# Optimization experiments

Hardware: AMD Instinct MI355X
Metric: run time of the kernel (lower is better)

## Reference

```python
import jax, jax.numpy as jnp
import numpy as np

BINS = 256


def _equalize_uint8(flat):
    """Torchvision-style histogram equalization.
    flat: int32 [BC, HW] with values in [0, 255]. Returns int32 [BC, HW]."""
    BC, HW = flat.shape
    # per-(image,channel) 256-bin histogram via one fused scatter-add
    ids = (flat + BINS * jnp.arange(BC, dtype=jnp.int32)[:, None]).reshape(-1)
    hist = jax.ops.segment_sum(
        jnp.ones((BC * HW,), dtype=jnp.int32), ids, num_segments=BC * BINS
    ).reshape(BC, BINS)
    # count in the last nonzero bin (torchvision: nonzero_hist[:-1].sum() = total - last)
    nz = hist > 0
    last_idx = (BINS - 1) - jnp.argmax(nz[:, ::-1], axis=1)
    last = jnp.take_along_axis(hist, last_idx[:, None], axis=1)[:, 0]
    step = (HW - last) // (BINS - 1)  # floor div by 255
    # lut = floor((cumsum(hist) + step//2) / step), shifted right by one, clamped
    cum = jnp.cumsum(hist, axis=1)
    safe_step = jnp.maximum(step, 1)[:, None]
    lut = (cum + (step // 2)[:, None]) // safe_step
    lut = jnp.clip(
        jnp.concatenate([jnp.zeros((BC, 1), jnp.int32), lut[:, :-1]], axis=1), 0, BINS - 1
    )
    eq = jnp.take_along_axis(lut, flat, axis=1)
    # step == 0 -> identity channel
    return jnp.where((step == 0)[:, None], flat, eq)


def setup_inputs() -> dict:
    key = jax.random.key(0)
    x = jax.random.uniform(key, (64, 3, 512, 512), dtype=jnp.float32)
    return {"x": x}


def reference(x) -> jnp.ndarray:
    B, C, H, W = x.shape
    # (x * 255).byte(): truncation toward zero == floor for non-negative inputs
    img = jnp.clip(jnp.floor(x * 255.0), 0.0, 255.0).astype(jnp.int32)
    flat = img.reshape(B * C, H * W)
    eq = _equalize_uint8(flat)
    return (eq.reshape(B, C, H, W).astype(x.dtype)) / 255.0
```

## Files before the change

kernel.cpp:

```cpp
#include <hip/hip_runtime.h>

#define BINS 256
#define HWPIX (512 * 512)
#define NCH 192
#define BPC 32
#define NBLK (NCH * BPC)

#define PWS_BYTES    ((size_t)NBLK * BINS * sizeof(int))
#define STAGED_BYTES ((size_t)NCH * HWPIX)

typedef float f4v __attribute__((ext_vector_type(4)));


__global__ __launch_bounds__(256) void hist_stage(const float* __restrict__ x,
                                                  int* __restrict__ pws,
                                                  uint4* __restrict__ staged4) {
    __shared__ int h[BINS];
    const int t = threadIdx.x;
    h[t] = 0;
    __syncthreads();

    const int ch  = blockIdx.x >> 5;
    const int blk = blockIdx.x & 31;
    const f4v* in4 = (const f4v*)(x + (size_t)ch * HWPIX);
    uint4* st4 = staged4 + (size_t)ch * (BPC * 512) + (size_t)blk * 512;
    const int idx0 = blk * 2048 + t;

#pragma unroll
    for (int j = 0; j < 2; ++j) {
        unsigned int p[4];
#pragma unroll
        for (int m = 0; m < 4; ++m) {
            const int k = idx0 + (4 * j + m) * 256;
            f4v v = in4[k];
            int b0 = (int)fminf(fmaxf(floorf(v.x * 255.0f), 0.0f), 255.0f);
            int b1 = (int)fminf(fmaxf(floorf(v.y * 255.0f), 0.0f), 255.0f);
            int b2 = (int)fminf(fmaxf(floorf(v.z * 255.0f), 0.0f), 255.0f);
            int b3 = (int)fminf(fmaxf(floorf(v.w * 255.0f), 0.0f), 255.0f);
            p[m] = (unsigned int)b0 | ((unsigned int)b1 << 8) |
                   ((unsigned int)b2 << 16) | ((unsigned int)b3 << 24);
            atomicAdd(&h[b0], 1);
            atomicAdd(&h[b1], 1);
            atomicAdd(&h[b2], 1);
            atomicAdd(&h[b3], 1);
        }
        uint4 w;
        w.x = p[0]; w.y = p[1]; w.z = p[2]; w.w = p[3];
        st4[j * 256 + t] = w;
    }
    __syncthreads();
    pws[(size_t)blockIdx.x * BINS + t] = h[t];
}

__global__ __launch_bounds__(256) void lut_kernel(const int* __restrict__ pws,
                                                  float* __restrict__ glut) {
    __shared__ int h[BINS];
    __shared__ int cum[BINS];
    __shared__ int red[BINS];
    const int t = threadIdx.x;
    const int ch = blockIdx.x;

    const int* base = pws + (size_t)ch * BPC * BINS;
    int s = 0;
#pragma unroll
    for (int b = 0; b < BPC; ++b) s += base[b * BINS + t];
    h[t]   = s;
    cum[t] = s;
    red[t] = (s > 0) ? t : -1;
    __syncthreads();

    for (int off = 128; off > 0; off >>= 1) {
        if (t < off) red[t] = max(red[t], red[t + off]);
        __syncthreads();
    }
    for (int off = 1; off < BINS; off <<= 1) {
        int v = cum[t];
        int a = (t >= off) ? cum[t - off] : 0;
        __syncthreads();
        cum[t] = v + a;
        __syncthreads();
    }

    const int last = h[red[0]];
    const int step = (HWPIX - last) / 255;
    int lutv;
    if (step == 0) {
        lutv = t;
    } else if (t == 0) {
        lutv = 0;
    } else {
        int val = (cum[t - 1] + (step >> 1)) / step;
        lutv = min(max(val, 0), 255);
    }
    glut[ch * BINS + t] = (float)lutv / 255.0f;
}

__global__ __launch_bounds__(256) void apply_staged(const uint4* __restrict__ staged4,
                                                    const float* __restrict__ glut,
                                                    float* __restrict__ out) {
    __shared__ float lutf[BINS];
    const int t = threadIdx.x;
    const int ch  = blockIdx.x >> 5;
    const int blk = blockIdx.x & 31;

    lutf[t] = glut[ch * BINS + t];
    __syncthreads();

    const uint4* st4 = staged4 + (size_t)ch * (BPC * 512) + (size_t)blk * 512;
    f4v* out4 = (f4v*)(out + (size_t)ch * HWPIX);
    const int idx0 = blk * 2048 + t;

#pragma unroll
    for (int j = 0; j < 2; ++j) {
        const uint4 w = st4[j * 256 + t];
        unsigned int p[4];
        p[0] = w.x; p[1] = w.y; p[2] = w.z; p[3] = w.w;
#pragma unroll
        for (int m = 0; m < 4; ++m) {
            const int k = idx0 + (4 * j + m) * 256;
            const unsigned int pm = p[m];
            f4v o;
            o.x = lutf[pm & 255u];
            o.y = lutf[(pm >> 8) & 255u];
            o.z = lutf[(pm >> 16) & 255u];
            o.w = lutf[pm >> 24];
            __builtin_nontemporal_store(o, &out4[k]);
        }
    }
}

extern "C" void kernel_launch(void* const* d_in, const int* in_sizes, int n_in,
                              void* d_out, int out_size, void* d_ws, size_t ws_size,
                              hipStream_t stream) {
    const float* x = (const float*)d_in[0];
    float* out = (float*)d_out;

    int* pws = (int*)d_ws;
    uint4* staged4 = (uint4*)((char*)d_ws + PWS_BYTES);
    float* glut = (float*)((char*)d_ws + PWS_BYTES + STAGED_BYTES);

    hist_stage  <<<NBLK, 256, 0, stream>>>(x, pws, staged4);
    lut_kernel  <<<NCH,  256, 0, stream>>>(pws, glut);
    apply_staged<<<NBLK, 256, 0, stream>>>(staged4, glut, out);
}
```

Before: 83.00 us.

## Fuse LUT computation into histogram kernel via last-block-done atomic counter

Per-block histograms are accumulated into a global per-channel histogram with atomics. The last block to finish for each channel, detected through an atomic ticket counter, computes the equalization LUT in the same kernel. This removes the separate LUT kernel launch and the partial-histogram workspace round trip. In exchange it adds a memset of counters and histograms, global atomic contention, and relies on memory ordering without an explicit fence.

```diff
diff --git a/kernel.cpp b/kernel.cpp
--- a/kernel.cpp
+++ b/kernel.cpp
@@ -6,16 +6,23 @@
 #define BPC 32
 #define NBLK (NCH * BPC)
 
-#define PWS_BYTES    ((size_t)NBLK * BINS * sizeof(int))
+#define FLAGS_BYTES  ((size_t)4096)
+#define GHIST_BYTES  ((size_t)NCH * BINS * sizeof(int))
 #define STAGED_BYTES ((size_t)NCH * HWPIX)
 
 typedef float f4v __attribute__((ext_vector_type(4)));
 
 
-__global__ __launch_bounds__(256) void hist_stage(const float* __restrict__ x,
-                                                  int* __restrict__ pws,
-                                                  uint4* __restrict__ staged4) {
+__global__ __launch_bounds__(256) void hist_stage_lut(const float* __restrict__ x,
+                                                      unsigned int* __restrict__ done,
+                                                      int* __restrict__ ghist,
+                                                      uint4* __restrict__ staged4,
+                                                      float* __restrict__ glut) {
     __shared__ int h[BINS];
+    __shared__ int cum[BINS];
+    __shared__ int red[BINS];
+    __shared__ unsigned int tick_s;
+
     const int t = threadIdx.x;
     h[t] = 0;
     __syncthreads();
@@ -49,50 +56,44 @@
         st4[j * 256 + t] = w;
     }
     __syncthreads();
-    pws[(size_t)blockIdx.x * BINS + t] = h[t];
-}
 
-__global__ __launch_bounds__(256) void lut_kernel(const int* __restrict__ pws,
-                                                  float* __restrict__ glut) {
-    __shared__ int h[BINS];
-    __shared__ int cum[BINS];
-    __shared__ int red[BINS];
-    const int t = threadIdx.x;
-    const int ch = blockIdx.x;
-
-    const int* base = pws + (size_t)ch * BPC * BINS;
-    int s = 0;
-#pragma unroll
-    for (int b = 0; b < BPC; ++b) s += base[b * BINS + t];
-    h[t]   = s;
-    cum[t] = s;
-    red[t] = (s > 0) ? t : -1;
+    atomicAdd(&ghist[ch * BINS + t], h[t]);
+    __syncthreads();
+    if (t == 0) tick_s = atomicAdd(&done[ch], 1u);
     __syncthreads();
 
-    for (int off = 128; off > 0; off >>= 1) {
-        if (t < off) red[t] = max(red[t], red[t + off]);
+    if (tick_s == BPC - 1) {
+        const int hv = atomicAdd(&ghist[ch * BINS + t], 0);
+        h[t]   = hv;
+        cum[t] = hv;
+        red[t] = (hv > 0) ? t : -1;
         __syncthreads();
+
+        for (int off = 128; off > 0; off >>= 1) {
+            if (t < off) red[t] = max(red[t], red[t + off]);
+            __syncthreads();
+        }
+        for (int off = 1; off < BINS; off <<= 1) {
+            int v = cum[t];
+            int a = (t >= off) ? cum[t - off] : 0;
+            __syncthreads();
+            cum[t] = v + a;
+            __syncthreads();
+        }
+
+        const int last = h[red[0]];
+        const int step = (HWPIX - last) / 255;
+        int lutv;
+        if (step == 0) {
+            lutv = t;
+        } else if (t == 0) {
+            lutv = 0;
+        } else {
+            int val = (cum[t - 1] + (step >> 1)) / step;
+            lutv = min(max(val, 0), 255);
+        }
+        glut[ch * BINS + t] = (float)lutv / 255.0f;
     }
-    for (int off = 1; off < BINS; off <<= 1) {
-        int v = cum[t];
-        int a = (t >= off) ? cum[t - off] : 0;
-        __syncthreads();
-        cum[t] = v + a;
-        __syncthreads();
-    }
-
-    const int last = h[red[0]];
-    const int step = (HWPIX - last) / 255;
-    int lutv;
-    if (step == 0) {
-        lutv = t;
-    } else if (t == 0) {
-        lutv = 0;
-    } else {
-        int val = (cum[t - 1] + (step >> 1)) / step;
-        lutv = min(max(val, 0), 255);
-    }
-    glut[ch * BINS + t] = (float)lutv / 255.0f;
 }
 
 __global__ __launch_bounds__(256) void apply_staged(const uint4* __restrict__ staged4,
@@ -135,11 +136,13 @@
     const float* x = (const float*)d_in[0];
     float* out = (float*)d_out;
 
-    int* pws = (int*)d_ws;
-    uint4* staged4 = (uint4*)((char*)d_ws + PWS_BYTES);
-    float* glut = (float*)((char*)d_ws + PWS_BYTES + STAGED_BYTES);
+    unsigned int* done = (unsigned int*)d_ws;
+    int* ghist = (int*)((char*)d_ws + FLAGS_BYTES);
+    uint4* staged4 = (uint4*)((char*)d_ws + FLAGS_BYTES + GHIST_BYTES);
+    float* glut = (float*)((char*)d_ws + FLAGS_BYTES + GHIST_BYTES + STAGED_BYTES);
 
-    hist_stage  <<<NBLK, 256, 0, stream>>>(x, pws, staged4);
-    lut_kernel  <<<NCH,  256, 0, stream>>>(pws, glut);
-    apply_staged<<<NBLK, 256, 0, stream>>>(staged4, glut, out);
+    hipMemsetAsync(d_ws, 0, FLAGS_BYTES + GHIST_BYTES, stream);
+
+    hist_stage_lut<<<NBLK, 256, 0, stream>>>(x, done, ghist, staged4, glut);
+    apply_staged  <<<NBLK, 256, 0, stream>>>(staged4, glut, out);
 }
```

New measurement: 96.32 us. 1.16x slower.
